# Optimization experiments

Hardware: AMD Instinct MI355X
Metric: run time of the kernel (lower is better)

The kernel has to match this reference:

```python
import jax, jax.numpy as jnp
import numpy as np

B = 262144
VD = 64          # vector_dim
N_ACTION = 8     # n_orientation + n_position
N_TYPE = 5
IN_DIM = 6 + N_ACTION  # (n_orientation + n_bounding_box) + n_action = 14


def _linear_init(k, fan_in, fan_out):
    k1, k2 = jax.random.split(k)
    s = 1.0 / np.sqrt(fan_in)
    W = jax.random.uniform(k1, (fan_in, fan_out), minval=-s, maxval=s, dtype=jnp.float32)
    b = jax.random.uniform(k2, (fan_out,), minval=-s, maxval=s, dtype=jnp.float32)
    return W, b


def setup_inputs() -> dict:
    key = jax.random.key(0)
    ks = jax.random.split(key, 12)
    W1, b1 = _linear_init(ks[0], IN_DIM, VD)
    W1b, b1b = _linear_init(ks[1], VD, VD)
    W1c, b1c = _linear_init(ks[2], VD, VD)
    W2a, b2a = _linear_init(ks[3], VD, N_ACTION)
    W2b, b2b = _linear_init(ks[4], VD, 1)
    Ta1, ta1 = _linear_init(ks[5], N_TYPE, VD)
    Ta2, ta2 = _linear_init(ks[6], VD, VD)
    Tb1, tb1 = _linear_init(ks[7], N_TYPE, VD)
    Tb2, tb2 = _linear_init(ks[8], VD, VD)
    states = jax.random.normal(ks[9], (B, 3, 18), dtype=jnp.float32)
    action = jax.random.normal(ks[10], (B, N_ACTION), dtype=jnp.float32)
    b_type = jax.random.normal(ks[11], (B, N_TYPE), dtype=jnp.float32)
    table = jnp.zeros((B, 6), dtype=jnp.float32)
    return dict(states=states, action=action, b_type=b_type, table=table,
                W1=W1, b1=b1, W1b=W1b, b1b=b1b, W1c=W1c, b1c=b1c,
                W2a=W2a, b2a=b2a, W2b=W2b, b2b=b2b,
                Ta1=Ta1, ta1=ta1, Ta2=Ta2, ta2=ta2,
                Tb1=Tb1, tb1=tb1, Tb2=Tb2, tb2=tb2)


def reference(states, action, b_type, table,
              W1, b1, W1b, b1b, W1c, b1c, W2a, b2a, W2b, b2b,
              Ta1, ta1, Ta2, ta2, Tb1, tb1, Tb2, tb2):
    def type_mlp(t, Wx, bx, Wy, by):  # Linear -> Tanh -> Linear -> Tanh
        return jnp.tanh(jnp.tanh(t @ Wx + bx) @ Wy + by)

    gate1 = type_mlp(b_type, Ta1, ta1, Ta2, ta2)  # [B, VD], type_a(b_type)

    # relative_positions: repeat action over n_blocks+1 slots, subtract block xy from first 3
    rel = jnp.tile(action[:, None, :], (1, 4, 1))          # [B, 4, 8]
    rel = rel.at[:, :3, :2].add(-states[:, :, :2])

    types = states[..., 13:18]                             # [B, 3, 5]
    st = states[..., 3:9]                                  # orientation+bbox slice, [B, 3, 6]

    def stack(x, g1):  # tanh(l1) -> tanh(l1b) -> *type_1 -> tanh(l1c)
        h = jnp.tanh(x @ W1 + b1)
        h = jnp.tanh(h @ W1b + b1b) * g1
        return jnp.tanh(h @ W1c + b1c)

    # table branch (no second type gating)
    h_t = stack(jnp.concatenate([rel[:, 3], table], axis=-1), gate1)  # [B, VD]
    w_t = jax.nn.sigmoid(h_t @ W2b + b2b)                             # [B, 1]
    v_t = h_t @ W2a + b2a                                             # [B, 8]

    # three neighbor branches, vectorized over the block axis
    xin = jnp.concatenate([rel[:, :3], st], axis=-1)       # [B, 3, 14]
    h = stack(xin, gate1[:, None, :])                      # [B, 3, VD]
    h = h * type_mlp(types, Tb1, tb1, Tb2, tb2)            # gate by type_b(types[:, i])
    w = jax.nn.sigmoid(h @ W2b + b2b)                      # [B, 3, 1]
    v = h @ W2a + b2a                                      # [B, 3, 8]

    mask = st[:, :, 0:1] != -1.0                           # [B, 3, 1]
    w = jnp.where(mask, w, 0.0)

    residuals = w_t * v_t + jnp.sum(w * v, axis=1)         # [B, 8]
    return residuals + action
```

## Files before the change

kernel.cpp:

```cpp
#include <hip/hip_runtime.h>

typedef unsigned int  uint;
typedef unsigned short u16;
typedef __attribute__((ext_vector_type(8))) short bf16x8;
typedef __attribute__((ext_vector_type(4))) float f32x4;

#define OF_W1B   0
#define OF_W1C   4096
#define OF_TA2   8192
#define OF_TB2   12288
#define OF_W1    16384
#define OF_TA1   18432
#define OF_TB1   20480
#define OF_W2AB  22528
#define WTOT     23552
#define BTA2 0
#define BTB2 64
#define BB1B 128
#define BB1C 192
#define BH   256
#define BIASN 272

#if defined(__has_builtin) && __has_builtin(__builtin_amdgcn_exp2f)
#define EXP2F(x) __builtin_amdgcn_exp2f(x)
#else
#define EXP2F(x) __expf((x) * 0.6931471805599453f)
#endif
#if defined(__has_builtin) && __has_builtin(__builtin_amdgcn_rcpf)
#define RCPF(x) __builtin_amdgcn_rcpf(x)
#else
#define RCPF(x) __fdividef(1.0f, (x))
#endif

__device__ __forceinline__ float ftanh(float x){
    const float e = EXP2F(x * 2.8853900817779268f);
    return __builtin_fmaf(-2.0f, RCPF(e + 1.0f), 1.0f);
}
__device__ __forceinline__ float fsigm(float x){
    return RCPF(1.0f + EXP2F(-1.4426950408889634f * x));
}
__device__ __forceinline__ uint cvtpk(float lo, float hi){
    uint r; asm("v_cvt_pk_bf16_f32 %0, %1, %2" : "=v"(r) : "v"(lo), "v"(hi)); return r;
}
__device__ __forceinline__ u16 bfb(float x){
    union { float f; uint u; } v; v.f = x;
    return (u16)((v.u + 0x7fffu + ((v.u >> 16) & 1u)) >> 16);
}
__device__ __forceinline__ f32x4 MFMA(bf16x8 a, bf16x8 b, f32x4 c){
    return __builtin_amdgcn_mfma_f32_16x16x32_bf16(a, b, c, 0, 0, 0);
}

__device__ __forceinline__ void zacc(f32x4 (&acc)[4][4]){
    #pragma unroll
    for (int mt = 0; mt < 4; ++mt)
        #pragma unroll
        for (int n = 0; n < 4; ++n) acc[mt][n] = f32x4{0.f, 0.f, 0.f, 0.f};
}
__device__ __forceinline__ void ld_bias(const float* BIAS, int bb, int q, f32x4 (&acc)[4][4]){
    #pragma unroll
    for (int mt = 0; mt < 4; ++mt){
        const f32x4 b4 = *(const f32x4*)&BIAS[bb + 16*mt + 4*q];
        #pragma unroll
        for (int n = 0; n < 4; ++n) acc[mt][n] = b4;
    }
}

__device__ __forceinline__ void layer_k32(const u16* Ab, const u16* Bb, int WB, f32x4 (&acc)[4][4]){
    bf16x8 A[4];
    #pragma unroll
    for (int mt = 0; mt < 4; ++mt) A[mt] = *(const bf16x8*)&Ab[WB + mt*512];
    #pragma unroll
    for (int n = 0; n < 4; ++n){
        const bf16x8 B = *(const bf16x8*)&Bb[n*1024];
        #pragma unroll
        for (int mt = 0; mt < 4; ++mt) acc[mt][n] = MFMA(A[mt], B, acc[mt][n]);
    }
}
__device__ __forceinline__ void layer_k64(const u16* Ab, const u16* Bb, int WB, f32x4 (&acc)[4][4]){
    #pragma unroll
    for (int s = 0; s < 2; ++s){
        bf16x8 A[4];
        #pragma unroll
        for (int mt = 0; mt < 4; ++mt) A[mt] = *(const bf16x8*)&Ab[WB + (mt*2+s)*512];
        #pragma unroll
        for (int n = 0; n < 4; ++n){
            const bf16x8 B = *(const bf16x8*)&Bb[n*1024 + s*512];
            #pragma unroll
            for (int mt = 0; mt < 4; ++mt) acc[mt][n] = MFMA(A[mt], B, acc[mt][n]);
        }
    }
}
__device__ __forceinline__ void head_k64(const u16* Ab, const u16* Bb, f32x4 (&ah)[4]){
    const bf16x8 A0 = *(const bf16x8*)&Ab[OF_W2AB];
    const bf16x8 A1 = *(const bf16x8*)&Ab[OF_W2AB + 512];
    #pragma unroll
    for (int n = 0; n < 4; ++n){
        const bf16x8 B0 = *(const bf16x8*)&Bb[n*1024];
        const bf16x8 B1 = *(const bf16x8*)&Bb[n*1024 + 512];
        ah[n] = MFMA(A0, B0, ah[n]);
        ah[n] = MFMA(A1, B1, ah[n]);
    }
}

__device__ __forceinline__ void stD(u16* EW, int mt, int n, uint lo, uint hi){
    *(uint2*)&EW[(n*2 + (mt>>1))*512 + (mt&1)*256] = make_uint2(lo, hi);
}
__device__ __forceinline__ void epi_tanh(u16* EW, const f32x4 (&acc)[4][4]){
    #pragma unroll
    for (int mt = 0; mt < 4; ++mt)
        #pragma unroll
        for (int n = 0; n < 4; ++n)
            stD(EW, mt, n, cvtpk(ftanh(acc[mt][n][0]), ftanh(acc[mt][n][1])),
                           cvtpk(ftanh(acc[mt][n][2]), ftanh(acc[mt][n][3])));
}

template<int NR>
__device__ __forceinline__ void write_xrow(u16* XW, const float (&x)[NR]){
    uint buf[16];
    #pragma unroll
    for (int i = 0; i < 16; ++i){
        if (2*i < NR){
            const float lo = x[2*i];
            const float hi = (2*i+1 < NR) ? x[2*i+1] : 0.f;
            buf[i] = cvtpk(lo, hi);
        } else buf[i] = 0u;
    }
    buf[15] = 0x3F800000u;
    #pragma unroll
    for (int kb = 0; kb < 4; ++kb)
        *(uint4*)&XW[kb*128] = make_uint4(buf[4*kb], buf[4*kb+1], buf[4*kb+2], buf[4*kb+3]);
}

__device__ __forceinline__ void stage_w64(u16* SHW, const float* __restrict__ Wg, int bb, int tid){
    #pragma unroll 1
    for (int idx = tid; idx < 4096; idx += 256){
        const int k = idx >> 6, j = idx & 63;
        SHW[bb + (((j>>4)<<1)|(k>>5))*512 + ((j&15)|(((k>>3)&3)<<4))*8 + (k&7)] = bfb(Wg[idx]);
    }
}

__global__ __launch_bounds__(256)
__attribute__((amdgpu_waves_per_eu(2, 2)))
void net_mfma(const float* __restrict__ states, const float* __restrict__ action,
              const float* __restrict__ b_type, const float* __restrict__ table,
              const float* __restrict__ W1,  const float* __restrict__ b1,
              const float* __restrict__ W1b, const float* __restrict__ b1b,
              const float* __restrict__ W1c, const float* __restrict__ b1c,
              const float* __restrict__ W2a, const float* __restrict__ b2a,
              const float* __restrict__ W2b, const float* __restrict__ b2b,
              const float* __restrict__ Ta1, const float* __restrict__ ta1,
              const float* __restrict__ Ta2, const float* __restrict__ ta2,
              const float* __restrict__ Tb1, const float* __restrict__ tb1,
              const float* __restrict__ Tb2, const float* __restrict__ tb2,
              float* __restrict__ out, int Btot)
{
    __shared__ u16   SHW[WTOT];
    __shared__ float BIAS[BIASN];
    __shared__ u16   ACT[4*4096];

    const int tid = threadIdx.x;

    { uint* z = (uint*)&SHW[OF_W1];
      #pragma unroll 1
      for (int i = tid; i < 3584; i += 256) z[i] = 0u; }
    __syncthreads();
    stage_w64(SHW, W1b, OF_W1B, tid);
    stage_w64(SHW, W1c, OF_W1C, tid);
    stage_w64(SHW, Ta2, OF_TA2, tid);
    stage_w64(SHW, Tb2, OF_TB2, tid);
    #pragma unroll 1
    for (int idx = tid; idx < 896; idx += 256){
        const int k = idx >> 6, j = idx & 63;
        SHW[OF_W1 + (j>>4)*512 + ((j&15)|(((k>>3)&3)<<4))*8 + (k&7)] = bfb(W1[idx]);
    }
    #pragma unroll 1
    for (int idx = tid; idx < 320; idx += 256){
        const int k = idx >> 6, j = idx & 63;
        const int d = (j>>4)*512 + ((j&15)|(((k>>3)&3)<<4))*8 + (k&7);
        SHW[OF_TA1 + d] = bfb(Ta1[idx]);
        SHW[OF_TB1 + d] = bfb(Tb1[idx]);
    }
    #pragma unroll 1
    for (int idx = tid; idx < 512; idx += 256){
        const int j = idx >> 3, i = idx & 7;
        SHW[OF_W2AB + (j>>5)*512 + (i|(((j>>3)&3)<<4))*8 + (j&7)] = bfb(W2a[idx]);
    }
    if (tid < 64){
        const int j = tid;
        SHW[OF_W2AB + (j>>5)*512 + (8|(((j>>3)&3)<<4))*8 + (j&7)] = bfb(W2b[j]);
        const int d31 = ((j&15)|(3<<4))*8 + 7;
        SHW[OF_W1  + (j>>4)*512 + d31] = bfb(b1[j]);
        SHW[OF_TA1 + (j>>4)*512 + d31] = bfb(ta1[j]);
        SHW[OF_TB1 + (j>>4)*512 + d31] = bfb(tb1[j]);
        BIAS[BTA2+j] = ta2[j]; BIAS[BTB2+j] = tb2[j];
        BIAS[BB1B+j] = b1b[j]; BIAS[BB1C+j] = b1c[j];
    }
    if (tid < 16) BIAS[BH+tid] = (tid < 8) ? b2a[tid] : (tid == 8 ? b2b[0] : 0.0f);
    __syncthreads();

    const int lane = tid & 63;
    const int q    = lane >> 4;
    const int wv   = tid >> 6;
    u16* ACW = &ACT[wv << 12];
    const u16* Ab = &SHW[lane*8];
    const u16* Bb = &ACW[lane*8];
    u16* XW = &ACW[(lane>>4)*1024 + (lane&15)*8];
    u16* EW = &ACW[(q>>1)*128 + (lane&15)*8 + 4*(q&1)];

    const int ebw   = blockIdx.x*256 + wv*64;
    const int elast = Btot - 1;
    const int eme   = min(ebw + lane, elast);

    float a8[8];
    { const float* ap = action + (size_t)eme*8;
      const float4 a0 = *(const float4*)ap; const float4 a1 = *(const float4*)(ap+4);
      a8[0]=a0.x; a8[1]=a0.y; a8[2]=a0.z; a8[3]=a0.w; a8[4]=a1.x; a8[5]=a1.y; a8[6]=a1.z; a8[7]=a1.w; }
    const float* sp = states + (size_t)eme*54;

    uint2 gp[4][4];
    {
        float x5[5];
        { const float* bp = b_type + (size_t)eme*5;
          #pragma unroll
          for (int k = 0; k < 5; ++k) x5[k] = bp[k]; }
        write_xrow<5>(XW, x5);
        f32x4 acc[4][4];
        zacc(acc);
        layer_k32(Ab, Bb, OF_TA1, acc);
        epi_tanh(EW, acc);
        ld_bias(BIAS, BTA2, q, acc);
        layer_k64(Ab, Bb, OF_TA2, acc);
        #pragma unroll
        for (int mt = 0; mt < 4; ++mt)
            #pragma unroll
            for (int n = 0; n < 4; ++n)
                gp[mt][n] = make_uint2(cvtpk(ftanh(acc[mt][n][0]), ftanh(acc[mt][n][1])),
                                       cvtpk(ftanh(acc[mt][n][2]), ftanh(acc[mt][n][3])));
    }

    f32x4 ro[4];
    #pragma unroll
    for (int n = 0; n < 4; ++n) ro[n] = f32x4{0.f, 0.f, 0.f, 0.f};

    #pragma unroll 1
    for (int r = 0; r < 4; ++r){
        const bool ht = (r < 3);
        uint2 tgp[4][4];
        f32x4 acc[4][4];

        if (ht){
            float xt[5];
            #pragma unroll
            for (int k = 0; k < 5; ++k) xt[k] = sp[r*18 + 13 + k];
            write_xrow<5>(XW, xt);
            zacc(acc);
            layer_k32(Ab, Bb, OF_TB1, acc);
            epi_tanh(EW, acc);
            ld_bias(BIAS, BTB2, q, acc);
            layer_k64(Ab, Bb, OF_TB2, acc);
            #pragma unroll
            for (int mt = 0; mt < 4; ++mt)
                #pragma unroll
                for (int n = 0; n < 4; ++n)
                    tgp[mt][n] = make_uint2(cvtpk(ftanh(acc[mt][n][0]), ftanh(acc[mt][n][1])),
                                            cvtpk(ftanh(acc[mt][n][2]), ftanh(acc[mt][n][3])));
        }

        float x14[14]; float maskf = 1.0f;
        #pragma unroll
        for (int k = 0; k < 8; ++k) x14[k] = a8[k];
        if (ht){
            x14[0] -= sp[r*18 + 0];
            x14[1] -= sp[r*18 + 1];
            #pragma unroll
            for (int k = 0; k < 6; ++k) x14[8 + k] = sp[r*18 + 3 + k];
            maskf = (x14[8] == -1.0f) ? 0.0f : 1.0f;
        } else {
            const float* tp = table + (size_t)eme*6;
            #pragma unroll
            for (int k = 0; k < 6; ++k) x14[8 + k] = tp[k];
        }
        write_xrow<14>(XW, x14);

        zacc(acc);
        layer_k32(Ab, Bb, OF_W1, acc);
        epi_tanh(EW, acc);

        ld_bias(BIAS, BB1B, q, acc);
        layer_k64(Ab, Bb, OF_W1B, acc);
        #pragma unroll
        for (int mt = 0; mt < 4; ++mt)
            #pragma unroll
            for (int n = 0; n < 4; ++n){
                const uint lo = gp[mt][n].x, hi = gp[mt][n].y;
                const float t0 = ftanh(acc[mt][n][0]) * __uint_as_float(lo << 16);
                const float t1 = ftanh(acc[mt][n][1]) * __uint_as_float(lo & 0xffff0000u);
                const float t2 = ftanh(acc[mt][n][2]) * __uint_as_float(hi << 16);
                const float t3 = ftanh(acc[mt][n][3]) * __uint_as_float(hi & 0xffff0000u);
                stD(EW, mt, n, cvtpk(t0, t1), cvtpk(t2, t3));
            }

        ld_bias(BIAS, BB1C, q, acc);
        layer_k64(Ab, Bb, OF_W1C, acc);
        #pragma unroll
        for (int mt = 0; mt < 4; ++mt)
            #pragma unroll
            for (int n = 0; n < 4; ++n){
                float m0 = 1.f, m1 = 1.f, m2 = 1.f, m3 = 1.f;
                if (ht){
                    const uint lo = tgp[mt][n].x, hi = tgp[mt][n].y;
                    m0 = __uint_as_float(lo << 16); m1 = __uint_as_float(lo & 0xffff0000u);
                    m2 = __uint_as_float(hi << 16); m3 = __uint_as_float(hi & 0xffff0000u);
                }
                stD(EW, mt, n, cvtpk(ftanh(acc[mt][n][0])*m0, ftanh(acc[mt][n][1])*m1),
                               cvtpk(ftanh(acc[mt][n][2])*m2, ftanh(acc[mt][n][3])*m3));
            }

        f32x4 ah[4];
        { const f32x4 b4 = *(const f32x4*)&BIAS[BH + 4*q];
          #pragma unroll
          for (int n = 0; n < 4; ++n) ah[n] = b4; }
        head_k64(Ab, Bb, ah);

        #pragma unroll
        for (int n = 0; n < 4; ++n){
            const float wm = fsigm(ah[n][0]);
            const float w  = __shfl(wm, 32 + (lane & 15), 64)
                           * __shfl(maskf, 16*n + (lane & 15), 64);
            #pragma unroll
            for (int c = 0; c < 4; ++c) ro[n][c] += w * ah[n][c];
        }
    }

    if (lane < 32){
        #pragma unroll
        for (int n = 0; n < 4; ++n){
            const int e2 = ebw + 16*n + (lane & 15);
            if (e2 < Btot){
                const int co = 4*q;
                const float4 av = *(const float4*)(action + (size_t)e2*8 + co);
                float4 res;
                res.x = av.x + ro[n][0]; res.y = av.y + ro[n][1];
                res.z = av.z + ro[n][2]; res.w = av.w + ro[n][3];
                *(float4*)(out + (size_t)e2*8 + co) = res;
            }
        }
    }
}

extern "C" void kernel_launch(void* const* d_in, const int* in_sizes, int n_in,
                              void* d_out, int out_size, void* d_ws, size_t ws_size,
                              hipStream_t stream)
{
    const float* states = (const float*)d_in[0];
    const float* action = (const float*)d_in[1];
    const float* b_type = (const float*)d_in[2];
    const float* table  = (const float*)d_in[3];
    const float* W1  = (const float*)d_in[4];
    const float* b1  = (const float*)d_in[5];
    const float* W1b = (const float*)d_in[6];
    const float* b1b = (const float*)d_in[7];
    const float* W1c = (const float*)d_in[8];
    const float* b1c = (const float*)d_in[9];
    const float* W2a = (const float*)d_in[10];
    const float* b2a = (const float*)d_in[11];
    const float* W2b = (const float*)d_in[12];
    const float* b2b = (const float*)d_in[13];
    const float* Ta1 = (const float*)d_in[14];
    const float* ta1 = (const float*)d_in[15];
    const float* Ta2 = (const float*)d_in[16];
    const float* ta2 = (const float*)d_in[17];
    const float* Tb1 = (const float*)d_in[18];
    const float* tb1 = (const float*)d_in[19];
    const float* Tb2 = (const float*)d_in[20];
    const float* tb2 = (const float*)d_in[21];
    float* out = (float*)d_out;

    const int Btot = in_sizes[1] / 8;
    const int grid = (Btot + 255) / 256;
    net_mfma<<<dim3(grid), dim3(256), 0, stream>>>(
        states, action, b_type, table,
        W1, b1, W1b, b1b, W1c, b1c, W2a, b2a, W2b, b2b,
        Ta1, ta1, Ta2, ta2, Tb1, tb1, Tb2, tb2,
        out, Btot);
}
```

Before: 122.2 us.

## Pre-swizzle weights in separate kernel and read them from global memory

Adds a small prep kernel that converts all weights and biases to the bf16 MFMA-swizzled layout once into a workspace buffer. The main kernel no longer stages weights into LDS per block; it reads A-fragments and biases straight from global memory (cached), shrinking LDS use and removing per-block staging and barriers. The waves-per-EU hint is raised to 4 to allow more occupancy. The risk is that weight fragments now come from L1/L2 instead of LDS on every layer, which may add latency to the inner MFMA loop.

Result: slower. 270.7 us (+121.4%).

```diff
diff --git a/kernel.cpp b/kernel.cpp
--- a/kernel.cpp
+++ b/kernel.cpp
@@ -56,16 +56,18 @@
         #pragma unroll
         for (int n = 0; n < 4; ++n) acc[mt][n] = f32x4{0.f, 0.f, 0.f, 0.f};
 }
-__device__ __forceinline__ void ld_bias(const float* BIAS, int bb, int q, f32x4 (&acc)[4][4]){
+__device__ __forceinline__ void ld_bias(const float* __restrict__ WB, int bb, int q,
+                                        f32x4 (&acc)[4][4]){
     #pragma unroll
     for (int mt = 0; mt < 4; ++mt){
-        const f32x4 b4 = *(const f32x4*)&BIAS[bb + 16*mt + 4*q];
+        const f32x4 b4 = *(const f32x4*)&WB[bb + 16*mt + 4*q];
         #pragma unroll
         for (int n = 0; n < 4; ++n) acc[mt][n] = b4;
     }
 }
 
-__device__ __forceinline__ void layer_k32(const u16* Ab, const u16* Bb, int WB, f32x4 (&acc)[4][4]){
+__device__ __forceinline__ void layer_k32(const u16* __restrict__ Ab, const u16* Bb, int WB,
+                                          f32x4 (&acc)[4][4]){
     bf16x8 A[4];
     #pragma unroll
     for (int mt = 0; mt < 4; ++mt) A[mt] = *(const bf16x8*)&Ab[WB + mt*512];
@@ -76,7 +78,8 @@
         for (int mt = 0; mt < 4; ++mt) acc[mt][n] = MFMA(A[mt], B, acc[mt][n]);
     }
 }
-__device__ __forceinline__ void layer_k64(const u16* Ab, const u16* Bb, int WB, f32x4 (&acc)[4][4]){
+__device__ __forceinline__ void layer_k64(const u16* __restrict__ Ab, const u16* Bb, int WB,
+                                          f32x4 (&acc)[4][4]){
     #pragma unroll
     for (int s = 0; s < 2; ++s){
         bf16x8 A[4];
@@ -90,7 +93,8 @@
         }
     }
 }
-__device__ __forceinline__ void head_k64(const u16* Ab, const u16* Bb, f32x4 (&ah)[4]){
+__device__ __forceinline__ void head_k64(const u16* __restrict__ Ab, const u16* Bb,
+                                         f32x4 (&ah)[4]){
     const bf16x8 A0 = *(const bf16x8*)&Ab[OF_W2AB];
     const bf16x8 A1 = *(const bf16x8*)&Ab[OF_W2AB + 512];
     #pragma unroll
@@ -131,78 +135,78 @@
         *(uint4*)&XW[kb*128] = make_uint4(buf[4*kb], buf[4*kb+1], buf[4*kb+2], buf[4*kb+3]);
 }
 
-__device__ __forceinline__ void stage_w64(u16* SHW, const float* __restrict__ Wg, int bb, int tid){
-    #pragma unroll 1
-    for (int idx = tid; idx < 4096; idx += 256){
-        const int k = idx >> 6, j = idx & 63;
-        SHW[bb + (((j>>4)<<1)|(k>>5))*512 + ((j&15)|(((k>>3)&3)<<4))*8 + (k&7)] = bfb(Wg[idx]);
-    }
-}
-
 __global__ __launch_bounds__(256)
-__attribute__((amdgpu_waves_per_eu(2, 2)))
-void net_mfma(const float* __restrict__ states, const float* __restrict__ action,
-              const float* __restrict__ b_type, const float* __restrict__ table,
-              const float* __restrict__ W1,  const float* __restrict__ b1,
-              const float* __restrict__ W1b, const float* __restrict__ b1b,
-              const float* __restrict__ W1c, const float* __restrict__ b1c,
-              const float* __restrict__ W2a, const float* __restrict__ b2a,
-              const float* __restrict__ W2b, const float* __restrict__ b2b,
-              const float* __restrict__ Ta1, const float* __restrict__ ta1,
-              const float* __restrict__ Ta2, const float* __restrict__ ta2,
-              const float* __restrict__ Tb1, const float* __restrict__ tb1,
-              const float* __restrict__ Tb2, const float* __restrict__ tb2,
-              float* __restrict__ out, int Btot)
+void prep_weights(const float* __restrict__ W1,  const float* __restrict__ b1,
+                  const float* __restrict__ W1b, const float* __restrict__ b1b,
+                  const float* __restrict__ W1c, const float* __restrict__ b1c,
+                  const float* __restrict__ W2a, const float* __restrict__ b2a,
+                  const float* __restrict__ W2b, const float* __restrict__ b2b,
+                  const float* __restrict__ Ta1, const float* __restrict__ ta1,
+                  const float* __restrict__ Ta2, const float* __restrict__ ta2,
+                  const float* __restrict__ Tb1, const float* __restrict__ tb1,
+                  const float* __restrict__ Tb2, const float* __restrict__ tb2,
+                  u16* __restrict__ WS)
 {
-    __shared__ u16   SHW[WTOT];
-    __shared__ float BIAS[BIASN];
-    __shared__ u16   ACT[4*4096];
-
-    const int tid = threadIdx.x;
-
-    { uint* z = (uint*)&SHW[OF_W1];
-      #pragma unroll 1
-      for (int i = tid; i < 3584; i += 256) z[i] = 0u; }
+    const int b = blockIdx.x, tid = threadIdx.x;
+    if (b < 4){
+        const float* Wg = (b==0) ? W1b : (b==1) ? W1c : (b==2) ? Ta2 : Tb2;
+        const int    bb = (b==0) ? OF_W1B : (b==1) ? OF_W1C : (b==2) ? OF_TA2 : OF_TB2;
+        #pragma unroll 1
+        for (int idx = tid; idx < 4096; idx += 256){
+            const int k = idx >> 6, j = idx & 63;
+            WS[bb + (((j>>4)<<1)|(k>>5))*512 + ((j&15)|(((k>>3)&3)<<4))*8 + (k&7)] = bfb(Wg[idx]);
+        }
+        return;
+    }
+    float* WB = (float*)(WS + WTOT);
+    #pragma unroll 1
+    for (int i = tid; i < (WTOT - OF_W1); i += 256) WS[OF_W1 + i] = 0;
     __syncthreads();
-    stage_w64(SHW, W1b, OF_W1B, tid);
-    stage_w64(SHW, W1c, OF_W1C, tid);
-    stage_w64(SHW, Ta2, OF_TA2, tid);
-    stage_w64(SHW, Tb2, OF_TB2, tid);
     #pragma unroll 1
     for (int idx = tid; idx < 896; idx += 256){
         const int k = idx >> 6, j = idx & 63;
-        SHW[OF_W1 + (j>>4)*512 + ((j&15)|(((k>>3)&3)<<4))*8 + (k&7)] = bfb(W1[idx]);
+        WS[OF_W1 + (j>>4)*512 + ((j&15)|(((k>>3)&3)<<4))*8 + (k&7)] = bfb(W1[idx]);
     }
     #pragma unroll 1
     for (int idx = tid; idx < 320; idx += 256){
         const int k = idx >> 6, j = idx & 63;
         const int d = (j>>4)*512 + ((j&15)|(((k>>3)&3)<<4))*8 + (k&7);
-        SHW[OF_TA1 + d] = bfb(Ta1[idx]);
-        SHW[OF_TB1 + d] = bfb(Tb1[idx]);
+        WS[OF_TA1 + d] = bfb(Ta1[idx]);
+        WS[OF_TB1 + d] = bfb(Tb1[idx]);
     }
     #pragma unroll 1
     for (int idx = tid; idx < 512; idx += 256){
         const int j = idx >> 3, i = idx & 7;
-        SHW[OF_W2AB + (j>>5)*512 + (i|(((j>>3)&3)<<4))*8 + (j&7)] = bfb(W2a[idx]);
+        WS[OF_W2AB + (j>>5)*512 + (i|(((j>>3)&3)<<4))*8 + (j&7)] = bfb(W2a[idx]);
     }
     if (tid < 64){
         const int j = tid;
-        SHW[OF_W2AB + (j>>5)*512 + (8|(((j>>3)&3)<<4))*8 + (j&7)] = bfb(W2b[j]);
+        WS[OF_W2AB + (j>>5)*512 + (8|(((j>>3)&3)<<4))*8 + (j&7)] = bfb(W2b[j]);
         const int d31 = ((j&15)|(3<<4))*8 + 7;
-        SHW[OF_W1  + (j>>4)*512 + d31] = bfb(b1[j]);
-        SHW[OF_TA1 + (j>>4)*512 + d31] = bfb(ta1[j]);
-        SHW[OF_TB1 + (j>>4)*512 + d31] = bfb(tb1[j]);
-        BIAS[BTA2+j] = ta2[j]; BIAS[BTB2+j] = tb2[j];
-        BIAS[BB1B+j] = b1b[j]; BIAS[BB1C+j] = b1c[j];
-    }
-    if (tid < 16) BIAS[BH+tid] = (tid < 8) ? b2a[tid] : (tid == 8 ? b2b[0] : 0.0f);
-    __syncthreads();
-
+        WS[OF_W1  + (j>>4)*512 + d31] = bfb(b1[j]);
+        WS[OF_TA1 + (j>>4)*512 + d31] = bfb(ta1[j]);
+        WS[OF_TB1 + (j>>4)*512 + d31] = bfb(tb1[j]);
+        WB[BTA2+j] = ta2[j]; WB[BTB2+j] = tb2[j];
+        WB[BB1B+j] = b1b[j]; WB[BB1C+j] = b1c[j];
+    }
+    if (tid < 16) WB[BH+tid] = (tid < 8) ? b2a[tid] : (tid == 8 ? b2b[0] : 0.0f);
+}
+
+__global__ __launch_bounds__(256)
+__attribute__((amdgpu_waves_per_eu(4)))
+void net_mfma(const float* __restrict__ states, const float* __restrict__ action,
+              const float* __restrict__ b_type, const float* __restrict__ table,
+              const u16* __restrict__ WS, int Btot, float* __restrict__ out)
+{
+    __shared__ u16 ACT[4*4096];
+
+    const int tid  = threadIdx.x;
     const int lane = tid & 63;
     const int q    = lane >> 4;
     const int wv   = tid >> 6;
     u16* ACW = &ACT[wv << 12];
-    const u16* Ab = &SHW[lane*8];
+    const u16*   Ab = &WS[lane*8];
+    const float* WB = (const float*)(WS + WTOT);
     const u16* Bb = &ACW[lane*8];
     u16* XW = &ACW[(lane>>4)*1024 + (lane&15)*8];
     u16* EW = &ACW[(q>>1)*128 + (lane&15)*8 + 4*(q&1)];
@@ -228,7 +232,7 @@
         zacc(acc);
         layer_k32(Ab, Bb, OF_TA1, acc);
         epi_tanh(EW, acc);
-        ld_bias(BIAS, BTA2, q, acc);
+        ld_bias(WB, BTA2, q, acc);
         layer_k64(Ab, Bb, OF_TA2, acc);
         #pragma unroll
         for (int mt = 0; mt < 4; ++mt)
@@ -256,7 +260,7 @@
             zacc(acc);
             layer_k32(Ab, Bb, OF_TB1, acc);
             epi_tanh(EW, acc);
-            ld_bias(BIAS, BTB2, q, acc);
+            ld_bias(WB, BTB2, q, acc);
             layer_k64(Ab, Bb, OF_TB2, acc);
             #pragma unroll
             for (int mt = 0; mt < 4; ++mt)
@@ -286,7 +290,7 @@
         layer_k32(Ab, Bb, OF_W1, acc);
         epi_tanh(EW, acc);
 
-        ld_bias(BIAS, BB1B, q, acc);
+        ld_bias(WB, BB1B, q, acc);
         layer_k64(Ab, Bb, OF_W1B, acc);
         #pragma unroll
         for (int mt = 0; mt < 4; ++mt)
@@ -300,7 +304,7 @@
                 stD(EW, mt, n, cvtpk(t0, t1), cvtpk(t2, t3));
             }
 
-        ld_bias(BIAS, BB1C, q, acc);
+        ld_bias(WB, BB1C, q, acc);
         layer_k64(Ab, Bb, OF_W1C, acc);
         #pragma unroll
         for (int mt = 0; mt < 4; ++mt)
@@ -317,7 +321,7 @@
             }
 
         f32x4 ah[4];
-        { const f32x4 b4 = *(const f32x4*)&BIAS[BH + 4*q];
+        { const f32x4 b4 = *(const f32x4*)&WB[BH + 4*q];
           #pragma unroll
           for (int n = 0; n < 4; ++n) ah[n] = b4; }
         head_k64(Ab, Bb, ah);
@@ -375,12 +379,13 @@
     const float* Tb2 = (const float*)d_in[20];
     const float* tb2 = (const float*)d_in[21];
     float* out = (float*)d_out;
+    u16* WS = (u16*)d_ws;
 
     const int Btot = in_sizes[1] / 8;
+    prep_weights<<<dim3(5), dim3(256), 0, stream>>>(
+        W1, b1, W1b, b1b, W1c, b1c, W2a, b2a, W2b, b2b,
+        Ta1, ta1, Ta2, ta2, Tb1, tb1, Tb2, tb2, WS);
     const int grid = (Btot + 255) / 256;
     net_mfma<<<dim3(grid), dim3(256), 0, stream>>>(
-        states, action, b_type, table,
-        W1, b1, W1b, b1b, W1c, b1c, W2a, b2a, W2b, b2b,
-        Ta1, ta1, Ta2, ta2, Tb1, tb1, Tb2, tb2,
-        out, Btot);
-}
+        states, action, b_type, table, WS, Btot, out);
+}
```
